# Optimization experiments

Hardware: AMD Instinct MI355X
Metric: run time of the kernel (lower is better)

## Reference

```python
import jax, jax.numpy as jnp
import numpy as np

N, D, H, C = 100000, 128, 8, 16  # nodes, units=H*C, heads, per-head channels
E = 400000                        # edges per edge set (2 edge sets)
LN_EPS = 1e-3                     # keras LayerNormalization default epsilon


def setup_inputs() -> dict:
    key = jax.random.key(0)
    ks = jax.random.split(key, 16)
    def dense(k, i, o):
        return jax.random.normal(k, (i, o), jnp.float32) / np.float32(np.sqrt(i))
    return dict(
        x=jax.random.normal(ks[0], (N, D), jnp.float32),
        src0=jax.random.randint(ks[1], (E,), 0, N),
        dst0=jax.random.randint(ks[2], (E,), 0, N),
        src1=jax.random.randint(ks[3], (E,), 0, N),
        dst1=jax.random.randint(ks[4], (E,), 0, N),
        Wk=dense(ks[5], D, D), bk=jnp.zeros((D,), jnp.float32),
        Wm=dense(ks[6], D, D), bm=jnp.zeros((D,), jnp.float32),
        Wq=dense(ks[7], D, D), bq=jnp.zeros((D,), jnp.float32),
        Wa=dense(ks[8], D, D), ba=jnp.zeros((D,), jnp.float32),
        Watt0=jax.random.normal(ks[9], (H, C, C), jnp.float32) / np.float32(np.sqrt(C)),
        Wmsg0=jax.random.normal(ks[10], (H, C, C), jnp.float32) / np.float32(np.sqrt(C)),
        Watt1=jax.random.normal(ks[11], (H, C, C), jnp.float32) / np.float32(np.sqrt(C)),
        Wmsg1=jax.random.normal(ks[12], (H, C, C), jnp.float32) / np.float32(np.sqrt(C)),
        prior0=jnp.ones((H,), jnp.float32),
        prior1=jnp.ones((H,), jnp.float32),
        skip=jnp.ones((), jnp.float32),
        gamma=jnp.ones((D,), jnp.float32),
        beta=jnp.zeros((D,), jnp.float32),
    )


def reference(x, src0, dst0, src1, dst1, Wk, bk, Wm, bm, Wq, bq, Wa, ba,
              Watt0, Wmsg0, Watt1, Wmsg1, prior0, prior1, skip, gamma, beta):
    # Node-level projections, split per head: [N, H, C]
    k = (x @ Wk + bk).reshape(N, H, C)
    m = (x @ Wm + bm).reshape(N, H, C)
    q = (x @ Wq + bq).reshape(N, H, C)
    scale = 1.0 / jnp.sqrt(jnp.float32(C))

    def edge_terms(src, dst, Watt, Wmsg, prior):
        # per-edge-type relation projections of gathered sender keys/messages
        ke = jnp.einsum('ehk,hkl->ehl', k[src], Watt)          # [E, H, C]
        score = jnp.einsum('ehl,ehl->eh', ke, q[dst]) * prior * scale  # [E, H]
        msg = jnp.einsum('ehk,hkl->ehl', m[src], Wmsg)          # [E, H, C]
        return score, msg

    s0, m0 = edge_terms(src0, dst0, Watt0, Wmsg0, prior0)
    s1, m1 = edge_terms(src1, dst1, Watt1, Wmsg1, prior1)

    # Joint segment softmax over all incoming edges (both edge sets) per receiver
    scores = jnp.concatenate([s0, s1], axis=0)   # [2E, H]
    msgs = jnp.concatenate([m0, m1], axis=0)     # [2E, H, C]
    recv = jnp.concatenate([dst0, dst1], axis=0)

    smax = jax.ops.segment_max(scores, recv, num_segments=N)   # [N, H]
    ex = jnp.exp(scores - smax[recv])
    denom = jax.ops.segment_sum(ex, recv, num_segments=N)      # [N, H]
    d_e = denom[recv]
    attn = ex / jnp.where(d_e > 0, d_e, 1.0)                   # [2E, H]

    pooled = jax.ops.segment_sum(attn[:, :, None] * msgs, recv,
                                 num_segments=N).reshape(N, D)  # [N, D]

    # aggr(gelu(pooled)); weighted skip; layer norm
    h = jax.nn.gelu(pooled, approximate=False) @ Wa + ba
    alpha = jax.nn.sigmoid(skip)
    out = alpha * h + (1.0 - alpha) * x
    mu = jnp.mean(out, axis=-1, keepdims=True)
    var = jnp.var(out, axis=-1, keepdims=True)
    out = (out - mu) * jax.lax.rsqrt(var + LN_EPS) * gamma + beta
    return out
```

## Files before the change

kernel.cpp:

```cpp
#include <hip/hip_runtime.h>
#include <hip/hip_bf16.h>
#include <math.h>

#define N_NODES 100000
#define DIM 128
#define NH 8
#define NC 16
#define E_EDGES 400000
#define LN_EPS 1e-3f
#define SCAN_B 1024
#define PROJ_GRID 512

typedef __attribute__((ext_vector_type(8))) short short8v;
typedef __attribute__((ext_vector_type(4))) short short4v;
typedef __attribute__((ext_vector_type(4))) float float4v;

__device__ __forceinline__ short bf16bits(float v) {
    __hip_bfloat16 b = __float2bfloat16(v);
    return *(short*)&b;
}

__device__ __forceinline__ void bf2x2(unsigned v, float& a, float& b) {
    a = __uint_as_float(v << 16);
    b = __uint_as_float(v & 0xffff0000u);
}

__global__ __launch_bounds__(128) void fuse_weights(
    const float* __restrict__ Wk, const float* __restrict__ bk,
    const float* __restrict__ Wm, const float* __restrict__ bm,
    const float* __restrict__ Wq, const float* __restrict__ bq,
    const float* __restrict__ Wa, const float* __restrict__ ba,
    const float* __restrict__ Watt0, const float* __restrict__ Wmsg0,
    const float* __restrict__ Watt1, const float* __restrict__ Wmsg1,
    const float* __restrict__ prior0, const float* __restrict__ prior1,
    __hip_bfloat16* __restrict__ Wt, float* __restrict__ bias)
{
    const int c = blockIdx.x;
    const int d = threadIdx.x;
    const int sec = c >> 7, j = c & 127, h = j >> 4, l = j & 15;
    float v, b;
    if (sec == 4)      { v = Wq[d * DIM + j]; b = bq[j]; }
    else if (sec == 5) { v = Wa[d * DIM + j]; b = ba[j]; }
    else {
        const float* W1 = (sec < 2) ? Wk : Wm;
        const float* bs = (sec < 2) ? bk : bm;
        const float* W2 = (sec == 0) ? Watt0 : (sec == 1) ? Watt1
                          : (sec == 2) ? Wmsg0 : Wmsg1;
        float scale = (sec == 0) ? prior0[h] * 0.25f
                    : (sec == 1) ? prior1[h] * 0.25f : 1.f;
        float s = 0.f, sb = 0.f;
        #pragma unroll
        for (int kk = 0; kk < NC; ++kk) {
            float w2 = W2[h * 256 + kk * 16 + l];
            s  = fmaf(W1[d * DIM + h * 16 + kk], w2, s);
            sb = fmaf(bs[h * 16 + kk], w2, sb);
        }
        v = s * scale; b = sb * scale;
    }
    Wt[(size_t)c * DIM + d] = __float2bfloat16(v);
    if (d == 0) bias[c] = b;
}

__global__ __launch_bounds__(512) void proj_mfma(
    const float* __restrict__ x,
    const __hip_bfloat16* __restrict__ Wt,
    const float* __restrict__ bias,
    __hip_bfloat16* __restrict__ km,
    __hip_bfloat16* __restrict__ qb)
{
    __shared__ __align__(16) short xs[2][32 * DIM];
    const int tid = threadIdx.x;
    const int wave = tid >> 6, lane = tid & 63;
    const int quad = lane >> 4, mcol = lane & 15;
    const int nt = N_NODES / 32;

    short8v wf[5][4];
    float4v bv[5];
    #pragma unroll
    for (int s = 0; s < 5; ++s) {
        const int c0 = s * 128 + wave * 16;
        const short* wp = (const short*)Wt + (size_t)(c0 + mcol) * DIM + quad * 8;
        #pragma unroll
        for (int kb = 0; kb < 4; ++kb)
            wf[s][kb] = *(const short8v*)(wp + kb * 32);
        bv[s] = *(const float4v*)(bias + c0 + quad * 4);
    }

    const int srow = tid >> 4, sc8 = tid & 15;
    const int swz = ((sc8 ^ (srow & 7)) * 8);

    int t = blockIdx.x;
    if (t >= nt) return;

    float4v f0 = *(const float4v*)(x + (size_t)(t * 32 + srow) * DIM + sc8 * 8);
    float4v f1 = *(const float4v*)(x + (size_t)(t * 32 + srow) * DIM + sc8 * 8 + 4);
    {
        short8v sv;
        #pragma unroll
        for (int j = 0; j < 4; ++j) { sv[j] = bf16bits(f0[j]); sv[j + 4] = bf16bits(f1[j]); }
        *(short8v*)(xs[0] + srow * DIM + swz) = sv;
    }
    {
        int nn = t + PROJ_GRID;
        if (nn < nt) {
            f0 = *(const float4v*)(x + (size_t)(nn * 32 + srow) * DIM + sc8 * 8);
            f1 = *(const float4v*)(x + (size_t)(nn * 32 + srow) * DIM + sc8 * 8 + 4);
        }
    }

    int cur = 0;
    for (; t < nt; t += PROJ_GRID) {
        __syncthreads();

        short8v b0[4], b1[4];
        #pragma unroll
        for (int kb = 0; kb < 4; ++kb) {
            const int ch = ((quad + kb * 4) ^ (mcol & 7)) * 8;
            b0[kb] = *(const short8v*)(xs[cur] + mcol * DIM + ch);
            b1[kb] = *(const short8v*)(xs[cur] + (mcol + 16) * DIM + ch);
        }

        const int r0 = t * 32;
        const int colb = wave * 32 + quad * 8;

        #pragma unroll
        for (int e = 0; e < 2; ++e) {
            float4v aK0 = {0.f,0.f,0.f,0.f}, aK1 = {0.f,0.f,0.f,0.f};
            float4v aM0 = {0.f,0.f,0.f,0.f}, aM1 = {0.f,0.f,0.f,0.f};
            #pragma unroll
            for (int kb = 0; kb < 4; ++kb) {
                aK0 = __builtin_amdgcn_mfma_f32_16x16x32_bf16(wf[e][kb],     b0[kb], aK0, 0, 0, 0);
                aK1 = __builtin_amdgcn_mfma_f32_16x16x32_bf16(wf[e][kb],     b1[kb], aK1, 0, 0, 0);
                aM0 = __builtin_amdgcn_mfma_f32_16x16x32_bf16(wf[2 + e][kb], b0[kb], aM0, 0, 0, 0);
                aM1 = __builtin_amdgcn_mfma_f32_16x16x32_bf16(wf[2 + e][kb], b1[kb], aM1, 0, 0, 0);
            }
            short8v o0, o1;
            #pragma unroll
            for (int g = 0; g < 4; ++g) {
                const int pos = (g & 2) * 2 + (g & 1);
                o0[pos]     = bf16bits(aK0[g] + bv[e][g]);
                o0[pos + 2] = bf16bits(aM0[g] + bv[2 + e][g]);
                o1[pos]     = bf16bits(aK1[g] + bv[e][g]);
                o1[pos + 2] = bf16bits(aM1[g] + bv[2 + e][g]);
            }
            short* dp = (short*)km
                      + ((size_t)(r0 + mcol) + (size_t)e * N_NODES) * 256 + colb;
            *(short8v*)dp              = o0;
            *(short8v*)(dp + 16 * 256) = o1;
        }

        {
            float4v a0v = {0.f,0.f,0.f,0.f}, a1v = {0.f,0.f,0.f,0.f};
            #pragma unroll
            for (int kb = 0; kb < 4; ++kb) {
                a0v = __builtin_amdgcn_mfma_f32_16x16x32_bf16(wf[4][kb], b0[kb], a0v, 0, 0, 0);
                a1v = __builtin_amdgcn_mfma_f32_16x16x32_bf16(wf[4][kb], b1[kb], a1v, 0, 0, 0);
            }
            short4v o0, o1;
            #pragma unroll
            for (int g = 0; g < 4; ++g) {
                o0[g] = bf16bits(a0v[g] + bv[4][g]);
                o1[g] = bf16bits(a1v[g] + bv[4][g]);
            }
            short* dp = (short*)qb + (size_t)(r0 + mcol) * DIM + wave * 16 + quad * 4;
            *(short4v*)dp              = o0;
            *(short4v*)(dp + 16 * DIM) = o1;
        }

        int nn = t + PROJ_GRID;
        if (nn < nt) {
            short8v sv;
            #pragma unroll
            for (int j = 0; j < 4; ++j) { sv[j] = bf16bits(f0[j]); sv[j + 4] = bf16bits(f1[j]); }
            *(short8v*)(xs[cur ^ 1] + srow * DIM + swz) = sv;
            int n2 = nn + PROJ_GRID;
            if (n2 < nt) {
                f0 = *(const float4v*)(x + (size_t)(n2 * 32 + srow) * DIM + sc8 * 8);
                f1 = *(const float4v*)(x + (size_t)(n2 * 32 + srow) * DIM + sc8 * 8 + 4);
            }
        }
        cur ^= 1;
    }
}

__global__ __launch_bounds__(256) void hist_kernel(
    const int* __restrict__ dst0, const int* __restrict__ dst1,
    int* __restrict__ counts)
{
    int e = blockIdx.x * 256 + threadIdx.x;
    if (e < E_EDGES) atomicAdd(&counts[dst0[e]], 1);
    int e1 = e - E_EDGES;
    if (e1 >= 0 && e1 < E_EDGES) atomicAdd(&counts[dst1[e1]], 1);
}

__global__ __launch_bounds__(SCAN_B) void scanA_kernel(
    const int* __restrict__ counts, int* __restrict__ row_ptr,
    int* __restrict__ bsum)
{
    __shared__ int buf[2][SCAN_B];
    int i = blockIdx.x * SCAN_B + threadIdx.x;
    int v = (i < N_NODES) ? counts[i] : 0;
    int cur = 0;
    buf[0][threadIdx.x] = v;
    __syncthreads();
    #pragma unroll
    for (int off = 1; off < SCAN_B; off <<= 1) {
        int t = buf[cur][threadIdx.x];
        int add = (threadIdx.x >= off) ? buf[cur][threadIdx.x - off] : 0;
        buf[cur ^ 1][threadIdx.x] = t + add;
        cur ^= 1;
        __syncthreads();
    }
    int inc = buf[cur][threadIdx.x];
    if (i < N_NODES) row_ptr[i] = inc - v;
    if (threadIdx.x == SCAN_B - 1) bsum[blockIdx.x] = inc;
}

__global__ __launch_bounds__(128) void scanB_kernel(int* __restrict__ bsum, int nblocks)
{
    __shared__ int buf[2][128];
    int t = threadIdx.x;
    int v = (t < nblocks) ? bsum[t] : 0;
    buf[0][t] = v;
    __syncthreads();
    int cur = 0;
    #pragma unroll
    for (int off = 1; off < 128; off <<= 1) {
        int a = buf[cur][t];
        if (t >= off) a += buf[cur][t - off];
        buf[cur ^ 1][t] = a;
        cur ^= 1;
        __syncthreads();
    }
    if (t < nblocks) bsum[t] = buf[cur][t] - v;
}

__global__ __launch_bounds__(SCAN_B) void scanC_kernel(
    int* __restrict__ row_ptr, int* __restrict__ cursor,
    const int* __restrict__ bsum)
{
    int i = blockIdx.x * SCAN_B + threadIdx.x;
    if (i < N_NODES) {
        int r = row_ptr[i] + bsum[blockIdx.x];
        row_ptr[i] = r;
        cursor[i] = r;
    }
}

__global__ __launch_bounds__(256) void scatter_kernel(
    const int* __restrict__ src0, const int* __restrict__ dst0,
    const int* __restrict__ src1, const int* __restrict__ dst1,
    int* __restrict__ cursor, unsigned int* __restrict__ eidx)
{
    int e = blockIdx.x * 256 + threadIdx.x;
    if (e < E_EDGES) {
        int d = dst0[e];
        int pos = atomicAdd(&cursor[d], 1);
        eidx[pos] = (unsigned int)src0[e];
    }
    int e1 = e - E_EDGES;
    if (e1 >= 0 && e1 < E_EDGES) {
        int d = dst1[e1];
        int pos = atomicAdd(&cursor[d], 1);
        eidx[pos] = (unsigned int)(src1[e1] + N_NODES);
    }
}

__global__ __launch_bounds__(256) void agg_kernel(
    const char* __restrict__ km,
    const unsigned* __restrict__ qv,
    const int* __restrict__ row_ptr, const int* __restrict__ counts,
    const unsigned int* __restrict__ eidx,
    unsigned int* __restrict__ pooled)
{
    const int wave = threadIdx.x >> 6, lane = threadIdx.x & 63;
    const int n = blockIdx.x * 4 + wave;
    if (n >= N_NODES) return;
    const int start = row_ptr[n], cnt = counts[n];
    const unsigned lane8 = (unsigned)lane << 3;

    unsigned qu = qv[(size_t)n * 64 + lane];
    float q0, q1; bf2x2(qu, q0, q1);

    float a0 = 0.f, a1 = 0.f, den = 0.f;

#define EDGE_ACC(u)                                                          \
    {                                                                        \
        float k0, k1, m0, m1;                                                \
        bf2x2((u).x, k0, k1); bf2x2((u).y, m0, m1);                          \
        float p = fmaf(k1, q1, k0 * q0);                                     \
        p += __shfl_xor(p, 1, 64);                                           \
        p += __shfl_xor(p, 2, 64);                                           \
        p += __shfl_xor(p, 4, 64);                                           \
        float e = __expf(p);                                                 \
        den += e;                                                            \
        a0 = fmaf(e, m0, a0); a1 = fmaf(e, m1, a1);                          \
    }

    int i = 0;
    for (; i + 4 <= cnt; i += 4) {
        unsigned r0i = eidx[start + i];
        unsigned r1i = eidx[start + i + 1];
        unsigned r2i = eidx[start + i + 2];
        unsigned r3i = eidx[start + i + 3];
        uint2 u0 = *(const uint2*)(km + ((r0i << 9) | lane8));
        uint2 u1 = *(const uint2*)(km + ((r1i << 9) | lane8));
        uint2 u2 = *(const uint2*)(km + ((r2i << 9) | lane8));
        uint2 u3 = *(const uint2*)(km + ((r3i << 9) | lane8));
        EDGE_ACC(u0); EDGE_ACC(u1); EDGE_ACC(u2); EDGE_ACC(u3);
    }
    for (; i < cnt; ++i) {
        unsigned r0i = eidx[start + i];
        uint2 u0 = *(const uint2*)(km + ((r0i << 9) | lane8));
        EDGE_ACC(u0);
    }
#undef EDGE_ACC

    float v0 = 0.f, v1 = 0.f;
    if (den > 0.f) {
        float inv = 1.f / den;
        v0 = a0 * inv; v1 = a1 * inv;
    }
    v0 = 0.5f * v0 * (1.f + erff(v0 * 0.70710678118654752f));
    v1 = 0.5f * v1 * (1.f + erff(v1 * 0.70710678118654752f));

    unsigned packed = ((unsigned)(unsigned short)bf16bits(v0))
                    | ((unsigned)(unsigned short)bf16bits(v1) << 16);
    pooled[(size_t)n * 64 + lane] = packed;
}

__global__ __launch_bounds__(256) void final_mfma(
    const __hip_bfloat16* __restrict__ pooled,
    const __hip_bfloat16* __restrict__ Wt,
    const float* __restrict__ bias,
    const float* __restrict__ x,
    const float* __restrict__ skip, const float* __restrict__ gamma,
    const float* __restrict__ beta, float* __restrict__ out)
{
    __shared__ float hs[32][DIM];
    const int wave = threadIdx.x >> 6, lane = threadIdx.x & 63;
    const int quad = lane >> 4, mcol = lane & 15;
    const int r0 = blockIdx.x * 32;

    short8v a0[4], a1[4];
    const short* pp0 = (const short*)pooled + (size_t)(r0 + mcol) * DIM + quad * 8;
    const short* pp1 = pp0 + 16 * DIM;
    #pragma unroll
    for (int kb = 0; kb < 4; ++kb) {
        a0[kb] = *(const short8v*)(pp0 + kb * 32);
        a1[kb] = *(const short8v*)(pp1 + kb * 32);
    }
    const float alpha = 1.f / (1.f + expf(-skip[0]));

    #pragma unroll
    for (int t = 0; t < 2; ++t) {
        const int c0 = wave * 32 + t * 16;
        const short* wp = (const short*)Wt + (size_t)(640 + c0 + mcol) * DIM + quad * 8;
        float4v acc0 = {0.f, 0.f, 0.f, 0.f};
        float4v acc1 = {0.f, 0.f, 0.f, 0.f};
        #pragma unroll
        for (int kb = 0; kb < 4; ++kb) {
            short8v bfr = *(const short8v*)(wp + kb * 32);
            acc0 = __builtin_amdgcn_mfma_f32_16x16x32_bf16(a0[kb], bfr, acc0, 0, 0, 0);
            acc1 = __builtin_amdgcn_mfma_f32_16x16x32_bf16(a1[kb], bfr, acc1, 0, 0, 0);
        }
        const float bcol = bias[640 + c0 + mcol];
        const int cc = c0 + mcol;
        const int rq = quad * 4;
        #pragma unroll
        for (int g = 0; g < 4; ++g) {
            int rA = rq + g, rB = rq + 16 + g;
            hs[rA][cc] = alpha * (acc0[g] + bcol)
                       + (1.f - alpha) * x[(size_t)(r0 + rA) * DIM + cc];
            hs[rB][cc] = alpha * (acc1[g] + bcol)
                       + (1.f - alpha) * x[(size_t)(r0 + rB) * DIM + cc];
        }
    }
    __syncthreads();

    float gam0 = gamma[lane], gam1 = gamma[lane + 64];
    float bet0 = beta[lane],  bet1 = beta[lane + 64];
    for (int r = wave; r < 32; r += 4) {
        int row = r0 + r;
        float v0 = hs[r][lane], v1 = hs[r][lane + 64];
        float s = v0 + v1, s2 = v0 * v0 + v1 * v1;
        #pragma unroll
        for (int off = 1; off < 64; off <<= 1) {
            s  += __shfl_xor(s,  off, 64);
            s2 += __shfl_xor(s2, off, 64);
        }
        float mu = s * (1.f / 128.f);
        float var = s2 * (1.f / 128.f) - mu * mu;
        float rstd = rsqrtf(var + LN_EPS);
        out[(size_t)row * DIM + lane]      = (v0 - mu) * rstd * gam0 + bet0;
        out[(size_t)row * DIM + lane + 64] = (v1 - mu) * rstd * gam1 + bet1;
    }
}

extern "C" void kernel_launch(void* const* d_in, const int* in_sizes, int n_in,
                              void* d_out, int out_size, void* d_ws, size_t ws_size,
                              hipStream_t stream) {
    const float* x     = (const float*)d_in[0];
    const int*   src0  = (const int*)d_in[1];
    const int*   dst0  = (const int*)d_in[2];
    const int*   src1  = (const int*)d_in[3];
    const int*   dst1  = (const int*)d_in[4];
    const float* Wk    = (const float*)d_in[5];
    const float* bk    = (const float*)d_in[6];
    const float* Wm    = (const float*)d_in[7];
    const float* bm    = (const float*)d_in[8];
    const float* Wq    = (const float*)d_in[9];
    const float* bq    = (const float*)d_in[10];
    const float* Wa    = (const float*)d_in[11];
    const float* ba    = (const float*)d_in[12];
    const float* Watt0 = (const float*)d_in[13];
    const float* Wmsg0 = (const float*)d_in[14];
    const float* Watt1 = (const float*)d_in[15];
    const float* Wmsg1 = (const float*)d_in[16];
    const float* prior0= (const float*)d_in[17];
    const float* prior1= (const float*)d_in[18];
    const float* skip  = (const float*)d_in[19];
    const float* gamma = (const float*)d_in[20];
    const float* beta  = (const float*)d_in[21];
    float* out = (float*)d_out;

    const size_t nd = (size_t)N_NODES * DIM;
    char* wsb = (char*)d_ws;
    __hip_bfloat16* Wt    = (__hip_bfloat16*)wsb;  wsb += (size_t)768 * DIM * 2;
    float* bias           = (float*)wsb;           wsb += 768 * 4;
    __hip_bfloat16* km    = (__hip_bfloat16*)wsb;  wsb += (size_t)2 * N_NODES * 256 * 2;
    __hip_bfloat16* qb    = (__hip_bfloat16*)wsb;  wsb += nd * 2;
    __hip_bfloat16* pooled= (__hip_bfloat16*)wsb;  wsb += nd * 2;
    int* counts  = (int*)wsb;                      wsb += (size_t)N_NODES * 4;
    int* row_ptr = (int*)wsb;                      wsb += (size_t)N_NODES * 4;
    int* cursor  = (int*)wsb;                      wsb += (size_t)N_NODES * 4;
    int* bsum    = (int*)wsb;                      wsb += 128 * 4;
    unsigned int* eidx = (unsigned int*)wsb;

    hipMemsetAsync(counts, 0, (size_t)N_NODES * 4, stream);

    const int scan_blocks = (N_NODES + SCAN_B - 1) / SCAN_B;
    const int edge_blocks = (2 * E_EDGES + 255) / 256;

    hist_kernel<<<dim3(edge_blocks), dim3(256), 0, stream>>>(dst0, dst1, counts);
    scanA_kernel<<<dim3(scan_blocks), dim3(SCAN_B), 0, stream>>>(counts, row_ptr, bsum);
    scanB_kernel<<<dim3(1), dim3(128), 0, stream>>>(bsum, scan_blocks);
    scanC_kernel<<<dim3(scan_blocks), dim3(SCAN_B), 0, stream>>>(row_ptr, cursor, bsum);
    scatter_kernel<<<dim3(edge_blocks), dim3(256), 0, stream>>>(
        src0, dst0, src1, dst1, cursor, eidx);

    fuse_weights<<<dim3(768), dim3(128), 0, stream>>>(
        Wk, bk, Wm, bm, Wq, bq, Wa, ba,
        Watt0, Wmsg0, Watt1, Wmsg1, prior0, prior1, Wt, bias);
    proj_mfma<<<dim3(PROJ_GRID), dim3(512), 0, stream>>>(
        x, Wt, bias, km, qb);

    agg_kernel<<<dim3((N_NODES + 3) / 4), dim3(256), 0, stream>>>(
        (const char*)km, (const unsigned*)qb, row_ptr, counts, eidx,
        (unsigned int*)pooled);

    final_mfma<<<dim3(N_NODES / 32), dim3(256), 0, stream>>>(
        pooled, Wt, bias, x, skip, gamma, beta, out);
}
```

Baseline: 357.4 us.

## Process two edges per wave with 16-byte gathers in aggregation kernel

Result: no change. 358.6 us (+0.3%).

```diff
diff --git a/kernel.cpp b/kernel.cpp
--- a/kernel.cpp
+++ b/kernel.cpp
@@ -121,7 +121,6 @@
         }
 
         const int r0 = t * 32;
-        const int colb = wave * 32 + quad * 8;
 
         #pragma unroll
         for (int e = 0; e < 2; ++e) {
@@ -137,14 +136,14 @@
             short8v o0, o1;
             #pragma unroll
             for (int g = 0; g < 4; ++g) {
-                const int pos = (g & 2) * 2 + (g & 1);
-                o0[pos]     = bf16bits(aK0[g] + bv[e][g]);
-                o0[pos + 2] = bf16bits(aM0[g] + bv[2 + e][g]);
-                o1[pos]     = bf16bits(aK1[g] + bv[e][g]);
-                o1[pos + 2] = bf16bits(aM1[g] + bv[2 + e][g]);
+                o0[g]     = bf16bits(aK0[g] + bv[e][g]);
+                o0[g + 4] = bf16bits(aM0[g] + bv[2 + e][g]);
+                o1[g]     = bf16bits(aK1[g] + bv[e][g]);
+                o1[g + 4] = bf16bits(aM1[g] + bv[2 + e][g]);
             }
             short* dp = (short*)km
-                      + ((size_t)(r0 + mcol) + (size_t)e * N_NODES) * 256 + colb;
+                      + ((size_t)(r0 + mcol) + (size_t)e * N_NODES) * 256
+                      + (wave * 4 + quad) * 8;
             *(short8v*)dp              = o0;
             *(short8v*)(dp + 16 * 256) = o1;
         }
@@ -268,65 +267,92 @@
 
 __global__ __launch_bounds__(256) void agg_kernel(
     const char* __restrict__ km,
-    const unsigned* __restrict__ qv,
+    const uint2* __restrict__ qv,
     const int* __restrict__ row_ptr, const int* __restrict__ counts,
     const unsigned int* __restrict__ eidx,
-    unsigned int* __restrict__ pooled)
+    uint2* __restrict__ pooled)
 {
     const int wave = threadIdx.x >> 6, lane = threadIdx.x & 63;
     const int n = blockIdx.x * 4 + wave;
     if (n >= N_NODES) return;
     const int start = row_ptr[n], cnt = counts[n];
-    const unsigned lane8 = (unsigned)lane << 3;
-
-    unsigned qu = qv[(size_t)n * 64 + lane];
-    float q0, q1; bf2x2(qu, q0, q1);
-
-    float a0 = 0.f, a1 = 0.f, den = 0.f;
-
-#define EDGE_ACC(u)                                                          \
+    const int hi = lane >> 5;
+    const int glane = lane & 31;
+    const unsigned g16 = (unsigned)glane << 4;
+
+    uint2 qu = qv[(size_t)n * 32 + glane];
+    float q0, q1, q2, q3;
+    bf2x2(qu.x, q0, q1); bf2x2(qu.y, q2, q3);
+
+    float a0 = 0.f, a1 = 0.f, a2 = 0.f, a3 = 0.f, den = 0.f;
+
+#define PAIR_ACC(u)                                                          \
     {                                                                        \
-        float k0, k1, m0, m1;                                                \
-        bf2x2((u).x, k0, k1); bf2x2((u).y, m0, m1);                          \
-        float p = fmaf(k1, q1, k0 * q0);                                     \
+        float k0, k1, k2, k3, m0, m1, m2, m3;                                \
+        bf2x2((u).x, k0, k1); bf2x2((u).y, k2, k3);                          \
+        bf2x2((u).z, m0, m1); bf2x2((u).w, m2, m3);                          \
+        float p = fmaf(k3, q3, fmaf(k2, q2, fmaf(k1, q1, k0 * q0)));         \
         p += __shfl_xor(p, 1, 64);                                           \
         p += __shfl_xor(p, 2, 64);                                           \
-        p += __shfl_xor(p, 4, 64);                                           \
         float e = __expf(p);                                                 \
         den += e;                                                            \
         a0 = fmaf(e, m0, a0); a1 = fmaf(e, m1, a1);                          \
+        a2 = fmaf(e, m2, a2); a3 = fmaf(e, m3, a3);                          \
     }
 
     int i = 0;
-    for (; i + 4 <= cnt; i += 4) {
-        unsigned r0i = eidx[start + i];
-        unsigned r1i = eidx[start + i + 1];
-        unsigned r2i = eidx[start + i + 2];
-        unsigned r3i = eidx[start + i + 3];
-        uint2 u0 = *(const uint2*)(km + ((r0i << 9) | lane8));
-        uint2 u1 = *(const uint2*)(km + ((r1i << 9) | lane8));
-        uint2 u2 = *(const uint2*)(km + ((r2i << 9) | lane8));
-        uint2 u3 = *(const uint2*)(km + ((r3i << 9) | lane8));
-        EDGE_ACC(u0); EDGE_ACC(u1); EDGE_ACC(u2); EDGE_ACC(u3);
-    }
-    for (; i < cnt; ++i) {
-        unsigned r0i = eidx[start + i];
-        uint2 u0 = *(const uint2*)(km + ((r0i << 9) | lane8));
-        EDGE_ACC(u0);
-    }
-#undef EDGE_ACC
-
-    float v0 = 0.f, v1 = 0.f;
-    if (den > 0.f) {
-        float inv = 1.f / den;
-        v0 = a0 * inv; v1 = a1 * inv;
-    }
-    v0 = 0.5f * v0 * (1.f + erff(v0 * 0.70710678118654752f));
-    v1 = 0.5f * v1 * (1.f + erff(v1 * 0.70710678118654752f));
-
-    unsigned packed = ((unsigned)(unsigned short)bf16bits(v0))
-                    | ((unsigned)(unsigned short)bf16bits(v1) << 16);
-    pooled[(size_t)n * 64 + lane] = packed;
+    for (; i + 8 <= cnt; i += 8) {
+        unsigned ra = eidx[start + i + hi];
+        unsigned rb = eidx[start + i + 2 + hi];
+        unsigned rc = eidx[start + i + 4 + hi];
+        unsigned rd = eidx[start + i + 6 + hi];
+        uint4 ua = *(const uint4*)(km + (((size_t)ra << 9) | g16));
+        uint4 ub = *(const uint4*)(km + (((size_t)rb << 9) | g16));
+        uint4 uc = *(const uint4*)(km + (((size_t)rc << 9) | g16));
+        uint4 ud = *(const uint4*)(km + (((size_t)rd << 9) | g16));
+        PAIR_ACC(ua); PAIR_ACC(ub); PAIR_ACC(uc); PAIR_ACC(ud);
+    }
+    for (; i + 2 <= cnt; i += 2) {
+        unsigned ra = eidx[start + i + hi];
+        uint4 ua = *(const uint4*)(km + (((size_t)ra << 9) | g16));
+        PAIR_ACC(ua);
+    }
+    if (i < cnt) {
+        unsigned ra = eidx[start + i];
+        uint4 ua = *(const uint4*)(km + (((size_t)ra << 9) | g16));
+        float k0, k1, k2, k3, m0, m1, m2, m3;
+        bf2x2(ua.x, k0, k1); bf2x2(ua.y, k2, k3);
+        bf2x2(ua.z, m0, m1); bf2x2(ua.w, m2, m3);
+        float p = fmaf(k3, q3, fmaf(k2, q2, fmaf(k1, q1, k0 * q0)));
+        p += __shfl_xor(p, 1, 64);
+        p += __shfl_xor(p, 2, 64);
+        float e = hi ? 0.f : __expf(p);
+        den += e;
+        a0 = fmaf(e, m0, a0); a1 = fmaf(e, m1, a1);
+        a2 = fmaf(e, m2, a2); a3 = fmaf(e, m3, a3);
+    }
+#undef PAIR_ACC
+
+    den += __shfl_xor(den, 32, 64);
+    a0 += __shfl_xor(a0, 32, 64);
+    a1 += __shfl_xor(a1, 32, 64);
+    a2 += __shfl_xor(a2, 32, 64);
+    a3 += __shfl_xor(a3, 32, 64);
+
+    float inv = (den > 0.f) ? (1.f / den) : 0.f;
+    float v0 = a0 * inv, v1 = a1 * inv, v2 = a2 * inv, v3 = a3 * inv;
+
+    float s0 = hi ? v2 : v0;
+    float s1 = hi ? v3 : v1;
+    s0 = 0.5f * s0 * (1.f + erff(s0 * 0.70710678118654752f));
+    s1 = 0.5f * s1 * (1.f + erff(s1 * 0.70710678118654752f));
+    unsigned pk = ((unsigned)(unsigned short)bf16bits(s0))
+                | ((unsigned)(unsigned short)bf16bits(s1) << 16);
+    unsigned ph = __shfl_xor(pk, 32, 64);
+    if (!hi) {
+        uint2 o; o.x = pk; o.y = ph;
+        pooled[(size_t)n * 32 + glane] = o;
+    }
 }
 
 __global__ __launch_bounds__(256) void final_mfma(
@@ -456,8 +482,8 @@
         x, Wt, bias, km, qb);
 
     agg_kernel<<<dim3((N_NODES + 3) / 4), dim3(256), 0, stream>>>(
-        (const char*)km, (const unsigned*)qb, row_ptr, counts, eidx,
-        (unsigned int*)pooled);
+        (const char*)km, (const uint2*)qb, row_ptr, counts, eidx,
+        (uint2*)pooled);
 
     final_mfma<<<dim3(N_NODES / 32), dim3(256), 0, stream>>>(
         pooled, Wt, bias, x, skip, gamma, beta, out);
```
